# Performance work log

Hardware: AMD Instinct MI355X
Metric: run time of the kernel (lower is better)

Reference implementation:

```python
import math
import jax, jax.numpy as jnp
import numpy as np

B, L, D, H, INNER = 8, 1024, 256, 8, 1024
HD = D // H
EPS = 1e-12


def _ln(x, g, b):
    m = jnp.mean(x, axis=-1, keepdims=True)
    v = jnp.mean((x - m) ** 2, axis=-1, keepdims=True)
    return (x - m) / jnp.sqrt(v + EPS) * g + b


def setup_inputs() -> dict:
    key = jax.random.key(0)
    ks = jax.random.split(key, 16)
    def lin(k, out_d, in_d):
        s = 1.0 / math.sqrt(in_d)
        kw, kb = jax.random.split(k)
        return (jax.random.uniform(kw, (out_d, in_d), jnp.float32, -s, s),
                jax.random.uniform(kb, (out_d,), jnp.float32, -s, s))
    Wq, bq = lin(ks[0], D, D)
    Wk, bk = lin(ks[1], D, D)
    Wv, bv = lin(ks[2], D, D)
    Wo, bo = lin(ks[3], D, D)
    W1, b1 = lin(ks[4], INNER, D)
    W2, b2 = lin(ks[5], D, INNER)
    return {
        'hidden_states': jax.random.normal(ks[6], (B, L, D), jnp.float32),
        'attention_mask': jnp.zeros((B, 1, 1, L), jnp.float32),
        'phi': jax.random.uniform(ks[7], (B, H, L), jnp.float32, 0.0, 2.0 * math.pi),
        'mag': jax.random.uniform(ks[8], (B, H, L), jnp.float32),
        'Wq': Wq, 'bq': bq, 'Wk': Wk, 'bk': bk, 'Wv': Wv, 'bv': bv,
        'Wo': Wo, 'bo': bo,
        'ln1_g': jnp.ones((D,), jnp.float32), 'ln1_b': jnp.zeros((D,), jnp.float32),
        'gamma': jnp.full((1, H, 1, 1), 0.1, jnp.float32),
        'W1': W1, 'b1': b1, 'W2': W2, 'b2': b2,
        'ln2_g': jnp.ones((D,), jnp.float32), 'ln2_b': jnp.zeros((D,), jnp.float32),
    }


def reference(hidden_states, attention_mask, phi, mag, Wq, bq, Wk, bk, Wv, bv,
              Wo, bo, ln1_g, ln1_b, gamma, W1, b1, W2, b2, ln2_g, ln2_b):
    residual = hidden_states
    def shape(x):  # [B,L,D] -> [B,H,L,hd]
        return x.reshape(B, L, H, HD).transpose(0, 2, 1, 3)
    q = shape(hidden_states @ Wq.T + bq)
    k = shape(hidden_states @ Wk.T + bk)
    v = shape(hidden_states @ Wv.T + bv)
    semantic = jnp.einsum('bhld,bhmd->bhlm', q, k) / math.sqrt(HD)
    # physics: gamma * (mag_i*mag_j) * cos(phi_i - phi_j), per band/head
    physics = gamma * (mag[..., :, None] * mag[..., None, :]) * jnp.cos(phi[..., :, None] - phi[..., None, :])
    scores = semantic + physics + attention_mask
    eye = jnp.eye(L, dtype=bool)[None, None]
    row_max = jnp.max(scores, axis=-1, keepdims=True)
    scores = jnp.where(row_max <= -1e8, jnp.where(eye, 0.0, scores), scores)
    probs = jax.nn.softmax(scores, axis=-1)
    ctx = jnp.einsum('bhlm,bhmd->bhld', probs, v).transpose(0, 2, 1, 3).reshape(B, L, D)
    attn_out = _ln(ctx @ Wo.T + bo + residual, ln1_g, ln1_b)
    h = attn_out @ W1.T + b1
    h = h * 0.5 * (1.0 + jax.lax.erf(h / math.sqrt(2.0)))  # exact-erf gelu as in source
    return _ln(h @ W2.T + b2 + attn_out, ln2_g, ln2_b)
```

## Files before the change

### kernel.cpp

```cpp
#include <hip/hip_runtime.h>
#include <hip/hip_bf16.h>
#include <math.h>

typedef __attribute__((ext_vector_type(8))) short bf16x8;
typedef __attribute__((ext_vector_type(4))) float f32x4;
typedef __attribute__((ext_vector_type(16))) float f32x16;

#define L2E 1.4426950408889634f

__device__ __forceinline__ unsigned short f2bf(float f) {
  union { float f; unsigned u; } v; v.f = f;
  unsigned r = v.u + 0x7fffu + ((v.u >> 16) & 1u);
  return (unsigned short)(r >> 16);
}
__device__ __forceinline__ unsigned pack2(float lo, float hi) {
  return (unsigned)f2bf(lo) | ((unsigned)f2bf(hi) << 16);
}
__device__ __forceinline__ float bf2f(unsigned short u) {
  union { unsigned u; float f; } v; v.u = ((unsigned)u) << 16; return v.f;
}
__device__ __forceinline__ float fexp2(float x) {
#if __has_builtin(__builtin_amdgcn_exp2f)
  return __builtin_amdgcn_exp2f(x);
#else
  return exp2f(x);
#endif
}
__device__ __forceinline__ unsigned cvtpk(float lo, float hi) {
  unsigned r;
  asm("v_cvt_pk_bf16_f32 %0, %1, %2" : "=v"(r) : "v"(lo), "v"(hi));
  return r;
}
__device__ __forceinline__ uint4 pack8(float4 a, float4 b) {
  return make_uint4(pack2(a.x, a.y), pack2(a.z, a.w), pack2(b.x, b.y),
                    pack2(b.z, b.w));
}
__device__ __forceinline__ void gload16(const void* gsrc, void* lds) {
  __builtin_amdgcn_global_load_lds(
      (const __attribute__((address_space(1))) unsigned int*)gsrc,
      (__attribute__((address_space(3))) unsigned int*)lds, 16, 0, 0);
}
#if __has_builtin(__builtin_amdgcn_permlane32_swap)
typedef __attribute__((ext_vector_type(2))) unsigned u32x2;
__device__ __forceinline__ void plswap(unsigned& a, unsigned& b) {
  u32x2 r = __builtin_amdgcn_permlane32_swap(a, b, false, false);
  a = r[0]; b = r[1];
}
#else
__device__ __forceinline__ void plswap(unsigned& a, unsigned& b) {
  unsigned as = (unsigned)__shfl_xor((int)a, 32, 64);
  unsigned bs = (unsigned)__shfl_xor((int)b, 32, 64);
  bool hi = (threadIdx.x & 32) != 0;
  unsigned na = hi ? bs : a;
  unsigned nb = hi ? b : as;
  a = na; b = nb;
}
#endif

__device__ __forceinline__ int xcd_swz(int p, int cpx) {
  return (p & 7) * cpx + (p >> 3);
}

__global__ __launch_bounds__(256) void gemm_qkv(
    const float* __restrict__ A, const float* __restrict__ Wq,
    const float* __restrict__ Wk, const float* __restrict__ Wv,
    const float* __restrict__ bq, const float* __restrict__ bk,
    const float* __restrict__ bv, const float* __restrict__ phi,
    const float* __restrict__ mag, const float* __restrict__ mask,
    const float* __restrict__ gamma, unsigned short* __restrict__ qx,
    unsigned short* __restrict__ kx, unsigned short* __restrict__ vt2) {
  const int tid = threadIdx.x;
  const int p = blockIdx.x;
  if (p >= 384) {
    const int bh = p - 384, b = bh >> 3, h = bh & 7;
    const float gm = gamma[h];
#pragma unroll
    for (int rr = 0; rr < 4; rr++) {
      int key = tid * 4 + rr;
      int row = bh * 1024 + key;
      float pp = phi[row], mg = mag[row];
      float sn, cs; sincosf(pp, &sn, &cs);
      float c = mg * cs, s = mg * sn;
      float msk = mask[b * 1024 + key];
      int ch = key >> 5, k32 = key & 31;
      size_t base = ((((size_t)(bh * 32 + ch) * 3 + 2) * 2 + 0) * 32 + k32) * 8;
      *(uint4*)&kx[base] = make_uint4(pack2(c, s), pack2(msk, 0.0f), 0u, 0u);
      *(uint4*)&kx[base + 256] = make_uint4(0u, 0u, 0u, 0u);
      *(uint4*)&qx[base] = make_uint4(pack2(L2E * gm * c, L2E * gm * s),
                                      pack2(L2E, 0.0f), 0u, 0u);
      *(uint4*)&qx[base + 256] = make_uint4(0u, 0u, 0u, 0u);
    }
    return;
  }
  __shared__ __align__(16) unsigned short As[128 * 64];
  __shared__ __align__(16) unsigned short Bs[128 * 64];
  const int w_id = xcd_swz(p, 48);
  const int xw = w_id % 6;
  const int mat = xw >> 1;
  const int n0 = (xw & 1) * 128;
  const int m0 = (w_id / 6) * 128;
  const float* W = (mat == 0) ? Wq : ((mat == 1) ? Wk : Wv);
  const float* bias = (mat == 0) ? bq : ((mat == 1) ? bk : bv);
  const int wm = (tid >> 7) & 1, wn = (tid >> 6) & 1;
  const int g = (tid >> 4) & 3, c = tid & 15;
  f32x4 acc[4][4] = {};
  for (int k0 = 0; k0 < 256; k0 += 64) {
    __syncthreads();
#pragma unroll
    for (int i = 0; i < 4; i++) {
      int idx = tid * 8 + i * 2048;
      int r = idx >> 6, c8 = idx & 63;
      const float* ap = &A[(size_t)(m0 + r) * 256 + k0 + c8];
      const float* wp = &W[(size_t)(n0 + r) * 256 + k0 + c8];
      float4 a0 = *(const float4*)ap, a1 = *(const float4*)(ap + 4);
      float4 w0 = *(const float4*)wp, w1 = *(const float4*)(wp + 4);
      int dst = r * 64 + (((c8 >> 3) ^ (r & 7)) << 3);
      *(uint4*)&As[dst] = pack8(a0, a1);
      *(uint4*)&Bs[dst] = pack8(w0, w1);
    }
    __syncthreads();
#pragma unroll
    for (int kk = 0; kk < 2; kk++) {
      bf16x8 af[4], bfr[4];
#pragma unroll
      for (int mi = 0; mi < 4; mi++) {
        int row = wm * 64 + mi * 16 + c;
        af[mi] = *(const bf16x8*)&As[row * 64 + (((g + 4 * kk) ^ (row & 7)) << 3)];
      }
#pragma unroll
      for (int ni = 0; ni < 4; ni++) {
        int row = wn * 64 + ni * 16 + c;
        bfr[ni] = *(const bf16x8*)&Bs[row * 64 + (((g + 4 * kk) ^ (row & 7)) << 3)];
      }
#pragma unroll
      for (int mi = 0; mi < 4; mi++)
#pragma unroll
        for (int ni = 0; ni < 4; ni++)
          acc[mi][ni] = __builtin_amdgcn_mfma_f32_16x16x32_bf16(af[mi], bfr[ni], acc[mi][ni], 0, 0, 0);
    }
  }
  const float scale = (mat == 0) ? (L2E * 0.17677669529663687f) : 1.0f;
#pragma unroll
  for (int ni = 0; ni < 4; ni++) {
    int n = n0 + wn * 64 + ni * 16 + c;
    float bv_ = bias[n];
    int h = n >> 5, dd = n & 31;
#pragma unroll
    for (int mi = 0; mi < 4; mi++) {
      int mbase = m0 + wm * 64 + mi * 16 + 4 * g;
      int bb = mbase >> 10, rowL = mbase & 1023;
      int bh = bb * 8 + h;
      if (mat < 2) {
        unsigned short* out = (mat == 0) ? qx : kx;
        int m_idx = dd >> 4, hi = (dd >> 3) & 1, j = dd & 7;
#pragma unroll
        for (int r = 0; r < 4; r++) {
          int keyL = rowL + r;
          int ch = keyL >> 5, k32 = keyL & 31;
          out[(((((size_t)bh * 32 + ch) * 3 + m_idx) * 2 + hi) * 32 + k32) * 8 + j] =
              f2bf((acc[mi][ni][r] + bv_) * scale);
        }
      } else {
        int keyL = rowL;
        int ch = keyL >> 5, t = (keyL >> 4) & 1, hi = (keyL >> 3) & 1;
        size_t base = (((((size_t)bh * 32 + ch) * 2 + t) * 2 + hi) * 32 + dd) * 8 + (g & 1) * 4;
        *(uint2*)&vt2[base] =
            make_uint2(pack2(acc[mi][ni][0] + bv_, acc[mi][ni][1] + bv_),
                       pack2(acc[mi][ni][2] + bv_, acc[mi][ni][3] + bv_));
      }
    }
  }
}

__global__ __launch_bounds__(256) void attn32(
    const unsigned short* __restrict__ qx, const unsigned short* __restrict__ kx,
    const unsigned short* __restrict__ vt2, unsigned short* __restrict__ ctx,
    const float* __restrict__ Wo, const float* __restrict__ W1,
    const float* __restrict__ W2, unsigned short* __restrict__ wts) {
  const int tid = threadIdx.x;
  const int p = blockIdx.x;
  if (p >= 512) {
    int i = (p - 512) * 1024 + tid * 4;
    const float* src; int off;
    if (i < 65536) { src = Wo; off = i; }
    else if (i < 327680) { src = W1; off = i - 65536; }
    else { src = W2; off = i - 327680; }
    float4 v = *(const float4*)&src[off];
    *(uint2*)&wts[i] = make_uint2(pack2(v.x, v.y), pack2(v.z, v.w));
    return;
  }
  const int wave = tid >> 6, lane = tid & 63;
  const int hi = lane >> 5, l31 = lane & 31;
  const int w_id = xcd_swz(p, 64);
  const int bh = w_id >> 3, bb = bh >> 3, h = bh & 7;
  const int qch = (w_id & 7) * 4 + wave;

  const size_t qoff = (((size_t)(bh * 32 + qch) * 3 * 2 + hi) * 32 + l31) * 8;
  bf16x8 qf0 = *(const bf16x8*)&qx[qoff];
  bf16x8 qf1 = *(const bf16x8*)&qx[qoff + 512];
  bf16x8 qf2 = *(const bf16x8*)&qx[qoff + 1024];

  f32x16 acc = {};
  float mrun = 0.0f, lsum = 0.0f;

  for (int ch = 0; ch < 32; ch++) {
    const size_t koff = (((size_t)(bh * 32 + ch) * 3 * 2 + hi) * 32 + l31) * 8;
    bf16x8 kf0 = *(const bf16x8*)&kx[koff];
    bf16x8 kf1 = *(const bf16x8*)&kx[koff + 512];
    bf16x8 kf2 = *(const bf16x8*)&kx[koff + 1024];
    const size_t voff = (((size_t)(bh * 32 + ch) * 2 * 2 + hi) * 32 + l31) * 8;
    bf16x8 vf0 = *(const bf16x8*)&vt2[voff];
    bf16x8 vf1 = *(const bf16x8*)&vt2[voff + 512];

    f32x16 s = {};
    __builtin_amdgcn_s_setprio(1);
    s = __builtin_amdgcn_mfma_f32_32x32x16_bf16(kf0, qf0, s, 0, 0, 0);
    s = __builtin_amdgcn_mfma_f32_32x32x16_bf16(kf1, qf1, s, 0, 0, 0);
    s = __builtin_amdgcn_mfma_f32_32x32x16_bf16(kf2, qf2, s, 0, 0, 0);
    __builtin_amdgcn_s_setprio(0);

    float pm = fmaxf(fmaxf(fmaxf(s[0], s[1]), fmaxf(s[2], s[3])),
                     fmaxf(fmaxf(s[4], s[5]), fmaxf(s[6], s[7])));
    pm = fmaxf(pm, fmaxf(fmaxf(fmaxf(s[8], s[9]), fmaxf(s[10], s[11])),
                         fmaxf(fmaxf(s[12], s[13]), fmaxf(s[14], s[15]))));
    pm = fmaxf(pm, __shfl_xor(pm, 32, 64));
    if (__any(pm > mrun + 12.0f)) {
      float mn = fmaxf(mrun, pm);
      float rs = fexp2(mrun - mn);
      lsum *= rs;
      mrun = mn;
#pragma unroll
      for (int r = 0; r < 16; r++) {
        float rr = __shfl(rs, (r & 3) + 8 * (r >> 2) + 4 * hi, 64);
        acc[r] *= rr;
      }
    }
    float pv[16];
#pragma unroll
    for (int r = 0; r < 16; r++) pv[r] = fexp2(s[r] - mrun);
    lsum += (((pv[0] + pv[1]) + (pv[2] + pv[3])) + ((pv[4] + pv[5]) + (pv[6] + pv[7]))) +
            (((pv[8] + pv[9]) + (pv[10] + pv[11])) + ((pv[12] + pv[13]) + (pv[14] + pv[15])));
    unsigned u0 = cvtpk(pv[0], pv[1]), u1 = cvtpk(pv[2], pv[3]);
    unsigned u2 = cvtpk(pv[4], pv[5]), u3 = cvtpk(pv[6], pv[7]);
    plswap(u0, u2); plswap(u1, u3);
    unsigned u4 = cvtpk(pv[8], pv[9]), u5 = cvtpk(pv[10], pv[11]);
    unsigned u6 = cvtpk(pv[12], pv[13]), u7 = cvtpk(pv[14], pv[15]);
    plswap(u4, u6); plswap(u5, u7);
    union { unsigned u[4]; bf16x8 v; } A1, A2;
    A1.u[0] = u0; A1.u[1] = u1; A1.u[2] = u2; A1.u[3] = u3;
    A2.u[0] = u4; A2.u[1] = u5; A2.u[2] = u6; A2.u[3] = u7;
    __builtin_amdgcn_s_setprio(1);
    acc = __builtin_amdgcn_mfma_f32_32x32x16_bf16(A1.v, vf0, acc, 0, 0, 0);
    acc = __builtin_amdgcn_mfma_f32_32x32x16_bf16(A2.v, vf1, acc, 0, 0, 0);
    __builtin_amdgcn_s_setprio(0);
  }
  lsum += __shfl_xor(lsum, 32, 64);
  float inv = 1.0f / lsum;
#pragma unroll
  for (int r = 0; r < 16; r++) {
    int qr = (r & 3) + 8 * (r >> 2) + 4 * hi;
    float rr = __shfl(inv, qr, 64);
    ctx[((size_t)bb * 1024 + qch * 32 + qr) * 256 + h * 32 + l31] = f2bf(acc[r] * rr);
  }
}

template <int KD, int RESBF, int OUTBF>
__global__ __launch_bounds__(512) void gemm_ln(
    const unsigned short* __restrict__ A, const unsigned short* __restrict__ W,
    const float* __restrict__ bias, const void* __restrict__ resid,
    const float* __restrict__ lng, const float* __restrict__ lnb,
    void* __restrict__ out) {
  __shared__ __align__(16) unsigned short As[16 * 64];
  __shared__ __align__(16) unsigned short Bs[256 * 64];
  __shared__ float red[2][8][16];
  const int tid = threadIdx.x;
  const int w_id = xcd_swz(blockIdx.x, 64);
  const int m0 = w_id * 16;
  const int w = tid >> 6, l = tid & 63;
  const int g = (l >> 4) & 3, c = l & 15;
  const int rr = l >> 3, scol = ((l & 7) ^ rr) << 3;
  const unsigned short* aSrc = &A[(size_t)(m0 + rr) * KD + scol];
  const unsigned short* bSrc = &W[(size_t)(w * 32 + rr) * KD + scol];
  unsigned short* bDst = &Bs[w * 32 * 64];
  f32x4 acc[2] = {};
  for (int k0 = 0; k0 < KD; k0 += 64) {
    __syncthreads();
    if (w == 0) {
      gload16(aSrc + k0, &As[0]);
      gload16(aSrc + (size_t)8 * KD + k0, &As[8 * 64]);
    }
#pragma unroll
    for (int i = 0; i < 4; i++)
      gload16(bSrc + (size_t)i * 8 * KD + k0, bDst + i * 8 * 64);
    __syncthreads();
#pragma unroll
    for (int kk = 0; kk < 2; kk++) {
      bf16x8 af = *(const bf16x8*)&As[c * 64 + (((g + 4 * kk) ^ (c & 7)) << 3)];
#pragma unroll
      for (int ni = 0; ni < 2; ni++) {
        int row = w * 32 + ni * 16 + c;
        bf16x8 bfr = *(const bf16x8*)&Bs[row * 64 + (((g + 4 * kk) ^ (row & 7)) << 3)];
        acc[ni] = __builtin_amdgcn_mfma_f32_16x16x32_bf16(af, bfr, acc[ni], 0, 0, 0);
      }
    }
  }
  float x[2][4], s1[4], s2[4];
#pragma unroll
  for (int r = 0; r < 4; r++) { s1[r] = 0.0f; s2[r] = 0.0f; }
#pragma unroll
  for (int ni = 0; ni < 2; ni++) {
    int n = w * 32 + ni * 16 + c;
    float bv_ = bias[n];
#pragma unroll
    for (int r = 0; r < 4; r++) {
      int m = m0 + 4 * g + r;
      float rv = RESBF
          ? bf2f(((const unsigned short*)resid)[(size_t)m * 256 + n])
          : ((const float*)resid)[(size_t)m * 256 + n];
      float v = acc[ni][r] + bv_ + rv;
      x[ni][r] = v;
      s1[r] += v;
      s2[r] += v * v;
    }
  }
#pragma unroll
  for (int off = 1; off < 16; off <<= 1) {
#pragma unroll
    for (int r = 0; r < 4; r++) {
      s1[r] += __shfl_xor(s1[r], off, 64);
      s2[r] += __shfl_xor(s2[r], off, 64);
    }
  }
  if (c == 0) {
#pragma unroll
    for (int r = 0; r < 4; r++) {
      red[0][w][4 * g + r] = s1[r];
      red[1][w][4 * g + r] = s2[r];
    }
  }
  __syncthreads();
#pragma unroll
  for (int r = 0; r < 4; r++) {
    int row = 4 * g + r;
    float t1 = 0.0f, t2 = 0.0f;
#pragma unroll
    for (int ww = 0; ww < 8; ww++) { t1 += red[0][ww][row]; t2 += red[1][ww][row]; }
    float mean = t1 * (1.0f / 256.0f);
    float var = fmaxf(t2 * (1.0f / 256.0f) - mean * mean, 0.0f);
    float istd = rsqrtf(var + 1e-12f);
    int m = m0 + row;
#pragma unroll
    for (int ni = 0; ni < 2; ni++) {
      int n = w * 32 + ni * 16 + c;
      float o = (x[ni][r] - mean) * istd * lng[n] + lnb[n];
      if constexpr (OUTBF)
        ((unsigned short*)out)[(size_t)m * 256 + n] = f2bf(o);
      else
        ((float*)out)[(size_t)m * 256 + n] = o;
    }
  }
}

__global__ __launch_bounds__(256) void gemm_ffn1(
    const unsigned short* __restrict__ A, const unsigned short* __restrict__ W,
    const float* __restrict__ bias, unsigned short* __restrict__ Cout,
    int N, int K) {
  __shared__ __align__(16) unsigned short As[128 * 64];
  __shared__ __align__(16) unsigned short Bs[128 * 64];
  const int tid = threadIdx.x;
  const int w_id = xcd_swz(blockIdx.x, 64);
  const int n0 = (w_id % 8) * 128;
  const int m0 = (w_id / 8) * 128;
  const int wm = (tid >> 7) & 1, wn = (tid >> 6) & 1;
  const int g = (tid >> 4) & 3, c = tid & 15;
  const int l = tid & 63, wv = tid >> 6;
  const int rr = l >> 3, scol = ((l & 7) ^ rr) << 3;
  const unsigned short* aSrc = &A[(size_t)(m0 + wv * 32 + rr) * K + scol];
  const unsigned short* bSrc = &W[(size_t)(n0 + wv * 32 + rr) * K + scol];
  unsigned short* aDst = &As[wv * 32 * 64];
  unsigned short* bDst = &Bs[wv * 32 * 64];
  f32x4 acc[4][4] = {};
  for (int k0 = 0; k0 < K; k0 += 64) {
    __syncthreads();
#pragma unroll
    for (int i = 0; i < 4; i++) {
      gload16(aSrc + (size_t)i * 8 * K + k0, aDst + i * 8 * 64);
      gload16(bSrc + (size_t)i * 8 * K + k0, bDst + i * 8 * 64);
    }
    __syncthreads();
#pragma unroll
    for (int kk = 0; kk < 2; kk++) {
      bf16x8 af[4], bfr[4];
#pragma unroll
      for (int mi = 0; mi < 4; mi++) {
        int row = wm * 64 + mi * 16 + c;
        af[mi] = *(const bf16x8*)&As[row * 64 + (((g + 4 * kk) ^ (row & 7)) << 3)];
      }
#pragma unroll
      for (int ni = 0; ni < 4; ni++) {
        int row = wn * 64 + ni * 16 + c;
        bfr[ni] = *(const bf16x8*)&Bs[row * 64 + (((g + 4 * kk) ^ (row & 7)) << 3)];
      }
#pragma unroll
      for (int mi = 0; mi < 4; mi++)
#pragma unroll
        for (int ni = 0; ni < 4; ni++)
          acc[mi][ni] = __builtin_amdgcn_mfma_f32_16x16x32_bf16(af[mi], bfr[ni], acc[mi][ni], 0, 0, 0);
    }
  }
#pragma unroll
  for (int ni = 0; ni < 4; ni++) {
    int n = n0 + wn * 64 + ni * 16 + c;
    float bv_ = bias[n];
#pragma unroll
    for (int mi = 0; mi < 4; mi++) {
      int mbase = m0 + wm * 64 + mi * 16 + 4 * g;
#pragma unroll
      for (int r = 0; r < 4; r++) {
        int m = mbase + r;
        float x = acc[mi][ni][r] + bv_;
        Cout[(size_t)m * N + n] =
            f2bf(x * 0.5f * (1.0f + erff(x * 0.70710678118654752f)));
      }
    }
  }
}

extern "C" void kernel_launch(void* const* d_in, const int* in_sizes, int n_in,
                              void* d_out, int out_size, void* d_ws,
                              size_t ws_size, hipStream_t stream) {
  const float* hs = (const float*)d_in[0];
  const float* mask = (const float*)d_in[1];
  const float* phi = (const float*)d_in[2];
  const float* mag = (const float*)d_in[3];
  const float* Wq = (const float*)d_in[4];
  const float* bq = (const float*)d_in[5];
  const float* Wk = (const float*)d_in[6];
  const float* bk = (const float*)d_in[7];
  const float* Wv = (const float*)d_in[8];
  const float* bv = (const float*)d_in[9];
  const float* Wo = (const float*)d_in[10];
  const float* bo = (const float*)d_in[11];
  const float* ln1g = (const float*)d_in[12];
  const float* ln1b = (const float*)d_in[13];
  const float* gamma = (const float*)d_in[14];
  const float* W1 = (const float*)d_in[15];
  const float* b1 = (const float*)d_in[16];
  const float* W2 = (const float*)d_in[17];
  const float* b2 = (const float*)d_in[18];
  const float* ln2g = (const float*)d_in[19];
  const float* ln2b = (const float*)d_in[20];

  char* wsb = (char*)d_ws;
  unsigned short* wts = (unsigned short*)(wsb + 0);
  unsigned short* ctx = (unsigned short*)(wsb + (6ull << 20));
  unsigned short* aout = (unsigned short*)(wsb + (10ull << 20));
  unsigned short* qx = (unsigned short*)(wsb + (22ull << 20));
  unsigned short* kx = (unsigned short*)(wsb + (28ull << 20));
  unsigned short* vt2 = (unsigned short*)(wsb + (34ull << 20));
  unsigned short* hbuf = (unsigned short*)(wsb + (40ull << 20));

  dim3 blk(256);
  gemm_qkv<<<dim3(448), blk, 0, stream>>>(hs, Wq, Wk, Wv, bq, bk, bv, phi,
                                          mag, mask, gamma, qx, kx, vt2);
  attn32<<<dim3(1088), blk, 0, stream>>>(qx, kx, vt2, ctx, Wo, W1, W2, wts);
  gemm_ln<256, 0, 1><<<dim3(512), dim3(512), 0, stream>>>(
      ctx, wts, bo, hs, ln1g, ln1b, aout);
  gemm_ffn1<<<dim3(512), blk, 0, stream>>>(aout, wts + 65536, b1, hbuf, 1024, 256);
  gemm_ln<1024, 1, 0><<<dim3(512), dim3(512), 0, stream>>>(
      hbuf, wts + 327680, b2, aout, ln2g, ln2b, d_out);
}
```

Measured before the change: 90.79 us.

## Double-buffer LDS tiles in gemm_ln and gemm_ffn1 to overlap loads with MFMA

Both GEMM kernels now use two LDS buffers. The next K-tile's global-to-LDS load is issued before computing on the current tile, which removes one barrier per iteration. gemm_ln also shrinks its K-tile from 64 to 32 with a new swizzle, and gemm_ffn1 hardcodes N=1024 and K=256 with a fully unrolled 4-step loop. The cost is twice the LDS per block, which may lower occupancy (gemm_ffn1 goes to 64KB), and more barriers per K in gemm_ln.

```diff
diff --git a/kernel.cpp b/kernel.cpp
--- a/kernel.cpp
+++ b/kernel.cpp
@@ -270,40 +270,42 @@
     const float* __restrict__ bias, const void* __restrict__ resid,
     const float* __restrict__ lng, const float* __restrict__ lnb,
     void* __restrict__ out) {
-  __shared__ __align__(16) unsigned short As[16 * 64];
-  __shared__ __align__(16) unsigned short Bs[256 * 64];
+  __shared__ __align__(16) unsigned short As[2][16 * 32];
+  __shared__ __align__(16) unsigned short Bs[2][256 * 32];
   __shared__ float red[2][8][16];
   const int tid = threadIdx.x;
   const int w_id = xcd_swz(blockIdx.x, 64);
   const int m0 = w_id * 16;
   const int w = tid >> 6, l = tid & 63;
   const int g = (l >> 4) & 3, c = l & 15;
-  const int rr = l >> 3, scol = ((l & 7) ^ rr) << 3;
-  const unsigned short* aSrc = &A[(size_t)(m0 + rr) * KD + scol];
-  const unsigned short* bSrc = &W[(size_t)(w * 32 + rr) * KD + scol];
-  unsigned short* bDst = &Bs[w * 32 * 64];
+  const int srow = l >> 2;
+  const int sgrp = ((l & 3) ^ (srow & 3)) << 3;
+  const unsigned short* aSrc = &A[(size_t)(m0 + srow) * KD + sgrp];
+  const unsigned short* bSrc = &W[(size_t)(w * 32 + srow) * KD + sgrp];
   f32x4 acc[2] = {};
-  for (int k0 = 0; k0 < KD; k0 += 64) {
+#define LN_STAGE(k0, b)                                                   \
+  {                                                                       \
+    if (w == 0) gload16(aSrc + (k0), &As[b][0]);                          \
+    gload16(bSrc + (k0), &Bs[b][(w * 32) * 32]);                          \
+    gload16(bSrc + (size_t)16 * KD + (k0), &Bs[b][(w * 32 + 16) * 32]);   \
+  }
+  LN_STAGE(0, 0);
+  __syncthreads();
+  const int gsw = (g ^ (c & 3)) << 3;
+  const int browbase = w * 32 + c;
+#pragma unroll 4
+  for (int t = 0; t < KD / 32; t++) {
+    const int cur = t & 1;
+    if (t < KD / 32 - 1) LN_STAGE((t + 1) * 32, cur ^ 1);
+    bf16x8 af = *(const bf16x8*)&As[cur][c * 32 + gsw];
+#pragma unroll
+    for (int ni = 0; ni < 2; ni++) {
+      bf16x8 bfr = *(const bf16x8*)&Bs[cur][(browbase + ni * 16) * 32 + gsw];
+      acc[ni] = __builtin_amdgcn_mfma_f32_16x16x32_bf16(af, bfr, acc[ni], 0, 0, 0);
+    }
     __syncthreads();
-    if (w == 0) {
-      gload16(aSrc + k0, &As[0]);
-      gload16(aSrc + (size_t)8 * KD + k0, &As[8 * 64]);
-    }
-#pragma unroll
-    for (int i = 0; i < 4; i++)
-      gload16(bSrc + (size_t)i * 8 * KD + k0, bDst + i * 8 * 64);
-    __syncthreads();
-#pragma unroll
-    for (int kk = 0; kk < 2; kk++) {
-      bf16x8 af = *(const bf16x8*)&As[c * 64 + (((g + 4 * kk) ^ (c & 7)) << 3)];
-#pragma unroll
-      for (int ni = 0; ni < 2; ni++) {
-        int row = w * 32 + ni * 16 + c;
-        bf16x8 bfr = *(const bf16x8*)&Bs[row * 64 + (((g + 4 * kk) ^ (row & 7)) << 3)];
-        acc[ni] = __builtin_amdgcn_mfma_f32_16x16x32_bf16(af, bfr, acc[ni], 0, 0, 0);
-      }
-    }
-  }
+  }
+#undef LN_STAGE
   float x[2][4], s1[4], s2[4];
 #pragma unroll
   for (int r = 0; r < 4; r++) { s1[r] = 0.0f; s2[r] = 0.0f; }
@@ -363,10 +365,9 @@
 
 __global__ __launch_bounds__(256) void gemm_ffn1(
     const unsigned short* __restrict__ A, const unsigned short* __restrict__ W,
-    const float* __restrict__ bias, unsigned short* __restrict__ Cout,
-    int N, int K) {
-  __shared__ __align__(16) unsigned short As[128 * 64];
-  __shared__ __align__(16) unsigned short Bs[128 * 64];
+    const float* __restrict__ bias, unsigned short* __restrict__ Cout) {
+  __shared__ __align__(16) unsigned short As[2][128 * 64];
+  __shared__ __align__(16) unsigned short Bs[2][128 * 64];
   const int tid = threadIdx.x;
   const int w_id = xcd_swz(blockIdx.x, 64);
   const int n0 = (w_id % 8) * 128;
@@ -375,31 +376,34 @@
   const int g = (tid >> 4) & 3, c = tid & 15;
   const int l = tid & 63, wv = tid >> 6;
   const int rr = l >> 3, scol = ((l & 7) ^ rr) << 3;
-  const unsigned short* aSrc = &A[(size_t)(m0 + wv * 32 + rr) * K + scol];
-  const unsigned short* bSrc = &W[(size_t)(n0 + wv * 32 + rr) * K + scol];
-  unsigned short* aDst = &As[wv * 32 * 64];
-  unsigned short* bDst = &Bs[wv * 32 * 64];
+  const unsigned short* aSrc = &A[(size_t)(m0 + wv * 32 + rr) * 256 + scol];
+  const unsigned short* bSrc = &W[(size_t)(n0 + wv * 32 + rr) * 256 + scol];
   f32x4 acc[4][4] = {};
-  for (int k0 = 0; k0 < K; k0 += 64) {
-    __syncthreads();
-#pragma unroll
-    for (int i = 0; i < 4; i++) {
-      gload16(aSrc + (size_t)i * 8 * K + k0, aDst + i * 8 * 64);
-      gload16(bSrc + (size_t)i * 8 * K + k0, bDst + i * 8 * 64);
-    }
-    __syncthreads();
+#define FFN1_STAGE(k0, b)                                                     \
+  {                                                                           \
+    _Pragma("unroll") for (int i = 0; i < 4; i++) {                           \
+      gload16(aSrc + (size_t)i * 8 * 256 + (k0), &As[b][wv * 2048 + i * 512]); \
+      gload16(bSrc + (size_t)i * 8 * 256 + (k0), &Bs[b][wv * 2048 + i * 512]); \
+    }                                                                         \
+  }
+  FFN1_STAGE(0, 0);
+  __syncthreads();
+#pragma unroll
+  for (int t = 0; t < 4; t++) {
+    const int cur = t & 1;
+    if (t < 3) FFN1_STAGE((t + 1) * 64, cur ^ 1);
 #pragma unroll
     for (int kk = 0; kk < 2; kk++) {
       bf16x8 af[4], bfr[4];
 #pragma unroll
       for (int mi = 0; mi < 4; mi++) {
         int row = wm * 64 + mi * 16 + c;
-        af[mi] = *(const bf16x8*)&As[row * 64 + (((g + 4 * kk) ^ (row & 7)) << 3)];
+        af[mi] = *(const bf16x8*)&As[cur][row * 64 + (((g + 4 * kk) ^ (row & 7)) << 3)];
       }
 #pragma unroll
       for (int ni = 0; ni < 4; ni++) {
         int row = wn * 64 + ni * 16 + c;
-        bfr[ni] = *(const bf16x8*)&Bs[row * 64 + (((g + 4 * kk) ^ (row & 7)) << 3)];
+        bfr[ni] = *(const bf16x8*)&Bs[cur][row * 64 + (((g + 4 * kk) ^ (row & 7)) << 3)];
       }
 #pragma unroll
       for (int mi = 0; mi < 4; mi++)
@@ -407,7 +411,9 @@
         for (int ni = 0; ni < 4; ni++)
           acc[mi][ni] = __builtin_amdgcn_mfma_f32_16x16x32_bf16(af[mi], bfr[ni], acc[mi][ni], 0, 0, 0);
     }
-  }
+    __syncthreads();
+  }
+#undef FFN1_STAGE
 #pragma unroll
   for (int ni = 0; ni < 4; ni++) {
     int n = n0 + wn * 64 + ni * 16 + c;
@@ -419,7 +425,7 @@
       for (int r = 0; r < 4; r++) {
         int m = mbase + r;
         float x = acc[mi][ni][r] + bv_;
-        Cout[(size_t)m * N + n] =
+        Cout[(size_t)m * 1024 + n] =
             f2bf(x * 0.5f * (1.0f + erff(x * 0.70710678118654752f)));
       }
     }
@@ -466,7 +472,7 @@
   attn32<<<dim3(1088), blk, 0, stream>>>(qx, kx, vt2, ctx, Wo, W1, W2, wts);
   gemm_ln<256, 0, 1><<<dim3(512), dim3(512), 0, stream>>>(
       ctx, wts, bo, hs, ln1g, ln1b, aout);
-  gemm_ffn1<<<dim3(512), blk, 0, stream>>>(aout, wts + 65536, b1, hbuf, 1024, 256);
+  gemm_ffn1<<<dim3(512), blk, 0, stream>>>(aout, wts + 65536, b1, hbuf);
   gemm_ln<1024, 1, 0><<<dim3(512), dim3(512), 0, stream>>>(
       hbuf, wts + 327680, b2, aout, ln2g, ln2b, d_out);
 }
```

New measurement: 95.61 us. 5.3% more time.
